# Kernel tuning notes

Hardware: AMD Instinct MI355X
Metric: run time of the kernel (lower is better)

Reference implementation:

```python
import jax, jax.numpy as jnp
import numpy as np

# Elliptical structuring-element sizes (cv2.MORPH_ELLIPSE-like), per init_kwargs.
KERNEL_SIZES = [3, 5, 7]
B, C, H, W = 16, 1, 1024, 1024
_MAX_VAL = 1e4  # kornia's max_val; geodesic border padding uses +-max_val
_EPS = 1e-7     # smp DiceLoss eps


def _ellipse_offsets(k):
    """Offsets (i, j) within a k x k window where the elliptical mask is 1."""
    r = k // 2
    yy, xx = np.mgrid[-r:r + 1, -r:r + 1]
    rr = max(r, 1)
    mask = (xx / rr) ** 2 + (yy / rr) ** 2 <= 1.0 + 1e-9
    return [(i, j) for i in range(k) for j in range(k) if mask[i, j]]


def _morph(x, k, offsets, is_dilation):
    """Flat morphological dilation (max) / erosion (min) over the ellipse support.
    Matches kornia's unfold-based morphology with geodesic border handling,
    but computed as a fused running max/min over static shifted views (no unfold blow-up)."""
    pad = k // 2
    fill = -_MAX_VAL if is_dilation else _MAX_VAL
    xp = jnp.pad(x, ((0, 0), (0, 0), (pad, pad), (pad, pad)), constant_values=fill)
    h, w = x.shape[-2], x.shape[-1]
    op = jnp.maximum if is_dilation else jnp.minimum
    i0, j0 = offsets[0]
    out = xp[..., i0:i0 + h, j0:j0 + w]
    for (i, j) in offsets[1:]:
        out = op(out, xp[..., i:i + h, j:j + w])
    return out


def _dice_loss(pred, target):
    """smp.losses.DiceLoss(mode='binary', from_logits=False): reduce over dims (batch, pixels)."""
    b = pred.shape[0]
    p = pred.reshape(b, 1, -1)
    t = target.reshape(b, 1, -1)
    inter = jnp.sum(p * t, axis=(0, 2))            # [1]
    card = jnp.sum(p + t, axis=(0, 2))             # [1]
    score = 2.0 * inter / jnp.clip(card, _EPS)
    loss = (1.0 - score) * (jnp.sum(t, axis=(0, 2)) > 0)
    return jnp.mean(loss)


def setup_inputs() -> dict:
    key = jax.random.key(0)
    k1, k2 = jax.random.split(key)
    pred = jax.random.uniform(k1, (B, C, H, W), dtype=jnp.float32)
    teacher = jax.random.uniform(k2, (B, C, H, W), dtype=jnp.float32)
    return {"pred_student_prob": pred, "teacher_prob": teacher}


def reference(pred_student_prob, teacher_prob):
    teacher = jax.lax.stop_gradient(teacher_prob)  # .detach()
    total = jnp.float32(0.0)
    for k in KERNEL_SIZES:
        offs = _ellipse_offsets(k)
        obj_dil = _morph(teacher, k, offs, True)
        obj_ero = _morph(teacher, k, offs, False)
        total = total + _dice_loss(pred_student_prob, obj_dil) + _dice_loss(pred_student_prob, obj_ero)
    return total / len(KERNEL_SIZES)
```

## Files before the change

kernel.cpp:

```cpp
#include <hip/hip_runtime.h>

#define H_ 1024
#define W_ 1024
#define B_ 16
#define TH 4
#define STEPS (TH + 6)
#define GX (H_ / TH)
#define NBLK (GX * B_)
#define NACC 13
#define TW 4
#define BT 256


__global__ __launch_bounds__(BT, 4) void k_partials(const float* __restrict__ pred,
                                                    const float* __restrict__ tch,
                                                    float* __restrict__ partials) {
  const int tid  = threadIdx.x;
  const int lane = tid & 63;
  const int n     = blockIdx.y * gridDim.x + blockIdx.x;
  const int b     = n >> 8;
  const int loc   = n & 255;
  const int ytile = (loc & 7) * 32 + (loc >> 3);
  const int y0    = ytile * TH;
  const int x0    = tid * TW;
  const float* tb = tch  + (size_t)b * (H_ * W_);
  const float* pb = pred + (size_t)b * (H_ * W_);

  float acc[NACC];
#pragma unroll
  for (int j = 0; j < NACC; j++) acc[j] = 0.f;

  float ring[7][10];
  const float* trp = nullptr;
  float4 pv, pvn;

#pragma unroll
  for (int s = 0; s < STEPS; ++s) {
    if (s >= 1) {
      const int sl = (s - 1) % 7;
      const float a3 = ring[sl][3], a4 = ring[sl][4], a5 = ring[sl][5], a6 = ring[sl][6];
      ring[sl][0] = __shfl_up(a4, 1, 64);
      ring[sl][1] = __shfl_up(a5, 1, 64);
      ring[sl][2] = __shfl_up(a6, 1, 64);
      ring[sl][7] = __shfl_down(a3, 1, 64);
      ring[sl][8] = __shfl_down(a4, 1, 64);
      ring[sl][9] = __shfl_down(a5, 1, 64);
      if (lane == 0) {
        if (tid > 0) {
          const float4 el = *reinterpret_cast<const float4*>(trp + x0 - 4);
          ring[sl][0] = el.y; ring[sl][1] = el.z; ring[sl][2] = el.w;
        } else {
          ring[sl][0] = ring[sl][1] = ring[sl][2] = a3;
        }
      }
      if (lane == 63) {
        if (tid < BT - 1) {
          const float4 er = *reinterpret_cast<const float4*>(trp + x0 + 4);
          ring[sl][7] = er.x; ring[sl][8] = er.y; ring[sl][9] = er.z;
        } else {
          ring[sl][7] = ring[sl][8] = ring[sl][9] = a6;
        }
      }
    }

    {
      const int t    = y0 + s - 3;
      const int trow = t < 0 ? 0 : (t >= H_ ? H_ - 1 : t);
      const float* tr = tb + (size_t)trow * W_;
      const float4 v  = *reinterpret_cast<const float4*>(tr + x0);
      const int sl = s % 7;
      ring[sl][3] = v.x; ring[sl][4] = v.y; ring[sl][5] = v.z; ring[sl][6] = v.w;
      trp = tr;
    }

    if (s == 5) pvn = *reinterpret_cast<const float4*>(pb + (size_t)y0 * W_ + x0);

    if (s >= 6) {
      pv = pvn;
      if (s < STEPS - 1)
        pvn = *reinterpret_cast<const float4*>(pb + (size_t)(y0 + s - 5) * W_ + x0);
      const float (&rm3)[10] = ring[(s - 6) % 7];
      const float (&rm2)[10] = ring[(s - 5) % 7];
      const float (&rm1)[10] = ring[(s - 4) % 7];
      const float (&rc )[10] = ring[(s - 3) % 7];
      const float (&rp1)[10] = ring[(s - 2) % 7];
      const float (&rp2)[10] = ring[(s - 1) % 7];
      const float (&rp3)[10] = ring[s % 7];
      const float p[TW] = {pv.x, pv.y, pv.z, pv.w};

      {
        float V3[10], V5[10];
#pragma unroll
        for (int i = 1; i <= 8; ++i) {
          V3[i] = fmaxf(fmaxf(rm1[i], rc[i]), rp1[i]);
          V5[i] = fmaxf(fmaxf(V3[i], rm2[i]), rp2[i]);
        }
#pragma unroll
        for (int c = 0; c < TW; ++c) {
          const int i = c + 3;
          const float V7 = fmaxf(fmaxf(V5[i], rm3[i]), rp3[i]);
          const float d3 = fmaxf(fmaxf(V3[i], rc[i - 1]), rc[i + 1]);
          float d5 = fmaxf(fmaxf(V5[i], V3[i - 1]), V3[i + 1]);
          d5 = fmaxf(fmaxf(d5, rc[i - 2]), rc[i + 2]);
          float d7 = fmaxf(fmaxf(V7, V5[i - 1]), V5[i + 1]);
          d7 = fmaxf(fmaxf(d7, V5[i - 2]), V5[i + 2]);
          d7 = fmaxf(fmaxf(d7, rc[i - 3]), rc[i + 3]);
          acc[0]  += p[c];
          acc[1]  += d3;  acc[2]  = fmaf(p[c], d3, acc[2]);
          acc[5]  += d5;  acc[6]  = fmaf(p[c], d5, acc[6]);
          acc[9]  += d7;  acc[10] = fmaf(p[c], d7, acc[10]);
        }
      }
      {
        float V3[10], V5[10];
#pragma unroll
        for (int i = 1; i <= 8; ++i) {
          V3[i] = fminf(fminf(rm1[i], rc[i]), rp1[i]);
          V5[i] = fminf(fminf(V3[i], rm2[i]), rp2[i]);
        }
#pragma unroll
        for (int c = 0; c < TW; ++c) {
          const int i = c + 3;
          const float V7 = fminf(fminf(V5[i], rm3[i]), rp3[i]);
          const float e3 = fminf(fminf(V3[i], rc[i - 1]), rc[i + 1]);
          float e5 = fminf(fminf(V5[i], V3[i - 1]), V3[i + 1]);
          e5 = fminf(fminf(e5, rc[i - 2]), rc[i + 2]);
          float e7 = fminf(fminf(V7, V5[i - 1]), V5[i + 1]);
          e7 = fminf(fminf(e7, V5[i - 2]), V5[i + 2]);
          e7 = fminf(fminf(e7, rc[i - 3]), rc[i + 3]);
          acc[3]  += e3;  acc[4]  = fmaf(p[c], e3, acc[4]);
          acc[7]  += e5;  acc[8]  = fmaf(p[c], e5, acc[8]);
          acc[11] += e7;  acc[12] = fmaf(p[c], e7, acc[12]);
        }
      }
    }
  }

#pragma unroll
  for (int j = 0; j < NACC; j++) {
    float v = acc[j];
#pragma unroll
    for (int off = 32; off > 0; off >>= 1) v += __shfl_down(v, off, 64);
    acc[j] = v;
  }
  __shared__ float red[4][NACC];
  const int wv = tid >> 6;
  if (lane == 0) {
#pragma unroll
    for (int j = 0; j < NACC; j++) red[wv][j] = acc[j];
  }
  __syncthreads();
  if (tid == 0) {
#pragma unroll
    for (int j = 0; j < NACC; j++)
      partials[j * NBLK + n] = red[0][j] + red[1][j] + red[2][j] + red[3][j];
  }
}

__global__ __launch_bounds__(256) void k_red(const float* __restrict__ partials,
                                             float* __restrict__ red13) {
  const int j   = blockIdx.x;
  const int tid = threadIdx.x;
  double a = 0.0;
#pragma unroll
  for (int k = 0; k < NBLK / 256; k++)
    a += (double)partials[j * NBLK + tid + k * 256];
#pragma unroll
  for (int off = 32; off > 0; off >>= 1) a += __shfl_down(a, off, 64);
  __shared__ double red[4];
  const int lane = tid & 63, wv = tid >> 6;
  if (lane == 0) red[wv] = a;
  __syncthreads();
  if (tid == 0) red13[j] = (float)0, red13[j] = (float)(red[0] + red[1] + red[2] + red[3]);
}

__global__ void k_final(const float* __restrict__ red13, float* __restrict__ out) {
  if (threadIdx.x == 0) {
    double t_[NACC];
#pragma unroll
    for (int j = 0; j < NACC; j++) t_[j] = (double)red13[j];
    const double Sp = t_[0];
    double total = 0.0;
#pragma unroll
    for (int k = 0; k < 3; k++) {
      const double Sd = t_[1 + 4 * k], Id = t_[2 + 4 * k];
      const double Se = t_[3 + 4 * k], Ie = t_[4 + 4 * k];
      double cd = Sp + Sd; if (cd < 1e-7) cd = 1e-7;
      double ce = Sp + Se; if (ce < 1e-7) ce = 1e-7;
      total += (1.0 - 2.0 * Id / cd) * (Sd > 0.0 ? 1.0 : 0.0);
      total += (1.0 - 2.0 * Ie / ce) * (Se > 0.0 ? 1.0 : 0.0);
    }
    out[0] = (float)(total / 3.0);
  }
}

extern "C" void kernel_launch(void* const* d_in, const int* in_sizes, int n_in,
                              void* d_out, int out_size, void* d_ws, size_t ws_size,
                              hipStream_t stream) {
  const float* pred = (const float*)d_in[0];
  const float* tch  = (const float*)d_in[1];
  float* partials = (float*)d_ws;
  float* red13    = (float*)d_ws + NACC * NBLK;

  k_partials<<<dim3(GX, B_), BT, 0, stream>>>(pred, tch, partials);
  k_red<<<NACC, 256, 0, stream>>>(partials, red13);
  k_final<<<1, 64, 0, stream>>>(red13, (float*)d_out);
}
```

Measured before the change: 156.0 us.

## Preload all teacher rows upfront and exchange wave edges through shared memory

```diff
diff --git a/kernel.cpp b/kernel.cpp
--- a/kernel.cpp
+++ b/kernel.cpp
@@ -17,6 +17,7 @@
                                                     float* __restrict__ partials) {
   const int tid  = threadIdx.x;
   const int lane = tid & 63;
+  const int wv   = tid >> 6;
   const int n     = blockIdx.y * gridDim.x + blockIdx.x;
   const int b     = n >> 8;
   const int loc   = n & 255;
@@ -26,67 +27,69 @@
   const float* tb = tch  + (size_t)b * (H_ * W_);
   const float* pb = pred + (size_t)b * (H_ * W_);
 
+  __shared__ float eL[4][STEPS][4], eR[4][STEPS][4];
+  __shared__ float redl[4][NACC];
+
+  float4 pv0 = *reinterpret_cast<const float4*>(pb + (size_t)y0 * W_ + x0);
+  float4 pv1 = *reinterpret_cast<const float4*>(pb + (size_t)(y0 + 1) * W_ + x0);
+  float4 row[STEPS];
+#pragma unroll
+  for (int s = 0; s < STEPS; ++s) {
+    const int t    = y0 + s - 3;
+    const int trow = t < 0 ? 0 : (t >= H_ ? H_ - 1 : t);
+    row[s] = *reinterpret_cast<const float4*>(tb + (size_t)trow * W_ + x0);
+  }
+#pragma unroll
+  for (int s = 0; s < STEPS; ++s) {
+    if (lane == 0)  { eL[wv][s][0] = row[s].x; eL[wv][s][1] = row[s].y;
+                      eL[wv][s][2] = row[s].z; eL[wv][s][3] = row[s].w; }
+    if (lane == 63) { eR[wv][s][0] = row[s].x; eR[wv][s][1] = row[s].y;
+                      eR[wv][s][2] = row[s].z; eR[wv][s][3] = row[s].w; }
+  }
+  __syncthreads();
+
   float acc[NACC];
 #pragma unroll
   for (int j = 0; j < NACC; j++) acc[j] = 0.f;
 
-  float ring[7][10];
-  const float* trp = nullptr;
-  float4 pv, pvn;
+  float ring[STEPS][10];
+  float4 pv2, pv3;
 
 #pragma unroll
   for (int s = 0; s < STEPS; ++s) {
-    if (s >= 1) {
-      const int sl = (s - 1) % 7;
-      const float a3 = ring[sl][3], a4 = ring[sl][4], a5 = ring[sl][5], a6 = ring[sl][6];
-      ring[sl][0] = __shfl_up(a4, 1, 64);
-      ring[sl][1] = __shfl_up(a5, 1, 64);
-      ring[sl][2] = __shfl_up(a6, 1, 64);
-      ring[sl][7] = __shfl_down(a3, 1, 64);
-      ring[sl][8] = __shfl_down(a4, 1, 64);
-      ring[sl][9] = __shfl_down(a5, 1, 64);
+    {
+      const float a3 = row[s].x, a4 = row[s].y, a5 = row[s].z, a6 = row[s].w;
+      ring[s][3] = a3; ring[s][4] = a4; ring[s][5] = a5; ring[s][6] = a6;
+      ring[s][0] = __shfl_up(a4, 1, 64);
+      ring[s][1] = __shfl_up(a5, 1, 64);
+      ring[s][2] = __shfl_up(a6, 1, 64);
+      ring[s][7] = __shfl_down(a3, 1, 64);
+      ring[s][8] = __shfl_down(a4, 1, 64);
+      ring[s][9] = __shfl_down(a5, 1, 64);
       if (lane == 0) {
-        if (tid > 0) {
-          const float4 el = *reinterpret_cast<const float4*>(trp + x0 - 4);
-          ring[sl][0] = el.y; ring[sl][1] = el.z; ring[sl][2] = el.w;
-        } else {
-          ring[sl][0] = ring[sl][1] = ring[sl][2] = a3;
-        }
+        if (wv > 0) { ring[s][0] = eR[wv - 1][s][1]; ring[s][1] = eR[wv - 1][s][2];
+                      ring[s][2] = eR[wv - 1][s][3]; }
+        else        { ring[s][0] = ring[s][1] = ring[s][2] = a3; }
       }
       if (lane == 63) {
-        if (tid < BT - 1) {
-          const float4 er = *reinterpret_cast<const float4*>(trp + x0 + 4);
-          ring[sl][7] = er.x; ring[sl][8] = er.y; ring[sl][9] = er.z;
-        } else {
-          ring[sl][7] = ring[sl][8] = ring[sl][9] = a6;
-        }
+        if (wv < 3) { ring[s][7] = eL[wv + 1][s][0]; ring[s][8] = eL[wv + 1][s][1];
+                      ring[s][9] = eL[wv + 1][s][2]; }
+        else        { ring[s][7] = ring[s][8] = ring[s][9] = a6; }
       }
     }
-
-    {
-      const int t    = y0 + s - 3;
-      const int trow = t < 0 ? 0 : (t >= H_ ? H_ - 1 : t);
-      const float* tr = tb + (size_t)trow * W_;
-      const float4 v  = *reinterpret_cast<const float4*>(tr + x0);
-      const int sl = s % 7;
-      ring[sl][3] = v.x; ring[sl][4] = v.y; ring[sl][5] = v.z; ring[sl][6] = v.w;
-      trp = tr;
-    }
-
-    if (s == 5) pvn = *reinterpret_cast<const float4*>(pb + (size_t)y0 * W_ + x0);
+    if (s == 4) pv2 = *reinterpret_cast<const float4*>(pb + (size_t)(y0 + 2) * W_ + x0);
+    if (s == 5) pv3 = *reinterpret_cast<const float4*>(pb + (size_t)(y0 + 3) * W_ + x0);
 
     if (s >= 6) {
-      pv = pvn;
-      if (s < STEPS - 1)
-        pvn = *reinterpret_cast<const float4*>(pb + (size_t)(y0 + s - 5) * W_ + x0);
-      const float (&rm3)[10] = ring[(s - 6) % 7];
-      const float (&rm2)[10] = ring[(s - 5) % 7];
-      const float (&rm1)[10] = ring[(s - 4) % 7];
-      const float (&rc )[10] = ring[(s - 3) % 7];
-      const float (&rp1)[10] = ring[(s - 2) % 7];
-      const float (&rp2)[10] = ring[(s - 1) % 7];
-      const float (&rp3)[10] = ring[s % 7];
-      const float p[TW] = {pv.x, pv.y, pv.z, pv.w};
+      const float (&rm3)[10] = ring[s - 6];
+      const float (&rm2)[10] = ring[s - 5];
+      const float (&rm1)[10] = ring[s - 4];
+      const float (&rc )[10] = ring[s - 3];
+      const float (&rp1)[10] = ring[s - 2];
+      const float (&rp2)[10] = ring[s - 1];
+      const float (&rp3)[10] = ring[s];
+      const float4 pvv = (s == 6) ? pv0 : (s == 7) ? pv1 : (s == 8) ? pv2 : pv3;
+      const float p[TW] = {pvv.x, pvv.y, pvv.z, pvv.w};
 
       {
         float V3[10], V5[10];
@@ -143,17 +146,15 @@
     for (int off = 32; off > 0; off >>= 1) v += __shfl_down(v, off, 64);
     acc[j] = v;
   }
-  __shared__ float red[4][NACC];
-  const int wv = tid >> 6;
   if (lane == 0) {
 #pragma unroll
-    for (int j = 0; j < NACC; j++) red[wv][j] = acc[j];
+    for (int j = 0; j < NACC; j++) redl[wv][j] = acc[j];
   }
   __syncthreads();
   if (tid == 0) {
 #pragma unroll
     for (int j = 0; j < NACC; j++)
-      partials[j * NBLK + n] = red[0][j] + red[1][j] + red[2][j] + red[3][j];
+      partials[j * NBLK + n] = redl[0][j] + redl[1][j] + redl[2][j] + redl[3][j];
   }
 }
 
@@ -171,7 +172,7 @@
   const int lane = tid & 63, wv = tid >> 6;
   if (lane == 0) red[wv] = a;
   __syncthreads();
-  if (tid == 0) red13[j] = (float)0, red13[j] = (float)(red[0] + red[1] + red[2] + red[3]);
+  if (tid == 0) red13[j] = (float)(red[0] + red[1] + red[2] + red[3]);
 }
 
 __global__ void k_final(const float* __restrict__ red13, float* __restrict__ out) {
```

New measurement: 147.9 us. 5.2% less time.
